# Performance work log

Hardware: AMD Instinct MI355X
Metric: run time of the kernel (lower is better)

Reference implementation:

```python
import jax, jax.numpy as jnp
import numpy as np

N_NODES = 50000
N_EDGES = 800000
H, D_IN, D_OUT = 4, 256, 64


def setup_inputs() -> dict:
    key = jax.random.key(0)
    ks = jax.random.split(key, 7)
    x = jax.random.normal(ks[0], (N_NODES, D_IN), dtype=jnp.float32)
    idx = jax.random.randint(ks[1], (2, N_EDGES), 0, N_NODES, dtype=jnp.int32)
    elem = jax.random.uniform(ks[2], (N_EDGES,), dtype=jnp.float32)
    Ws = jax.random.normal(ks[3], (H, D_IN, D_OUT), dtype=jnp.float32) * 0.05
    bs = jax.random.normal(ks[4], (H, D_OUT), dtype=jnp.float32) * 0.05
    aw = jax.random.normal(ks[5], (H, 2 * D_OUT + 1), dtype=jnp.float32) * 0.05
    ab = jax.random.normal(ks[6], (H,), dtype=jnp.float32) * 0.05
    return {"x": x, "idx": idx, "elem": elem, "Ws": Ws, "bs": bs, "aw": aw, "ab": ab}


def reference(x, idx, elem, Ws, bs, aw, ab):
    N = x.shape[0]
    O = Ws.shape[-1]
    # per-head MLP (num_mlp_layers=1 -> single Linear): [H, N, O]
    feats = jnp.einsum('nd,hdo->hno', x, Ws) + bs[:, None, :]
    # attention linear on concat(src, dst, elem): split weights instead of
    # materializing the [E, 2O+1] concat; math is identical.
    aw_src, aw_dst, aw_e = aw[:, :O], aw[:, O:2 * O], aw[:, 2 * O]
    a_s = jnp.einsum('hno,ho->hn', feats, aw_src)   # [H, N]
    a_d = jnp.einsum('hno,ho->hn', feats, aw_dst)   # [H, N]
    src, dst = idx[0], idx[1]
    score = a_s[:, src] + a_d[:, dst] + aw_e[:, None] * elem[None, :] + ab[:, None]
    w = jnp.exp(-jax.nn.relu(score / 20.0))        # [H, E], in (0, 1]
    dst_f = feats[:, dst]                          # [H, E, O] gather
    seg = lambda vals: jax.ops.segment_sum(vals, src, num_segments=N)
    pooled = jax.vmap(lambda wi, fi: seg(wi[:, None] * fi))(w, dst_f)  # [H, N, O]
    row_sum = jax.vmap(lambda wi: seg(wi))(w)                          # [H, N]
    out = pooled / row_sum[:, :, None]
    # concat heads along feature dim: [N, H*O]
    return jnp.transpose(out, (1, 0, 2)).reshape(N, H * O)
```

## Files before the change

kernel.cpp:

```cpp
#include <hip/hip_runtime.h>
#include <math.h>

constexpr int DIN = 256;
constexpr int H   = 4;
constexpr int O   = 64;
constexpr int HO  = H * O;
constexpr int AWS = 2 * O + 1;

typedef __bf16 bf16x8 __attribute__((ext_vector_type(8)));
typedef __bf16 bf16x4 __attribute__((ext_vector_type(4)));
typedef float  f32x4  __attribute__((ext_vector_type(4)));

__device__ __forceinline__ float bf2f(unsigned short u) {
    union { unsigned int i; float f; } c;
    c.i = ((unsigned int)u) << 16;
    return c.f;
}

__global__ __launch_bounds__(256) void k_prep(const float* __restrict__ Ws,
    __bf16* __restrict__ Bt, int* __restrict__ cnt, int N)
{
    const int b = blockIdx.x;
    if (b < 256) {
        const int i = b * 256 + threadIdx.x;
        const int k = i & 255;
        const int n = i >> 8;
        Bt[n * 256 + k] = (__bf16)Ws[(n >> 6) * (DIN * O) + k * O + (n & 63)];
    } else {
        const int i = (b - 256) * 256 + threadIdx.x;
        if (i < N) cnt[i] = 0;
    }
}

__global__ __launch_bounds__(256) void k_gemm_hist(const float* __restrict__ x,
    const __bf16* __restrict__ Bt, const float* __restrict__ bs,
    const float* __restrict__ aw, int N, int GB,
    __bf16* __restrict__ F, float* __restrict__ a_sT, float* __restrict__ a_dT,
    const int* __restrict__ idx, int E, int* __restrict__ cnt,
    int* __restrict__ rank)
{
    __shared__ __bf16 As[64][DIN + 8];
    const int b = blockIdx.x;
    const int t = threadIdx.x;

    if (b >= GB) {
        const int base_e = (b - GB) * 1024 + t;
        #pragma unroll
        for (int i = 0; i < 4; ++i) {
            const int e = base_e + i * 256;
            if (e < E) rank[e] = atomicAdd(&cnt[idx[e]], 1);
        }
        return;
    }

    const int w    = t >> 6;
    const int lane = t & 63;
    const int c15  = lane & 15;
    const int quad = lane >> 4;
    const int n0   = b * 64;

    #pragma unroll
    for (int i = 0; i < 16; ++i) {
        const int r   = i * 4 + w;
        const int row = n0 + r;
        float4 xv = make_float4(0.f, 0.f, 0.f, 0.f);
        if (row < N) xv = *(const float4*)&x[(size_t)row * DIN + lane * 4];
        bf16x4 pv = { (__bf16)xv.x, (__bf16)xv.y, (__bf16)xv.z, (__bf16)xv.w };
        *(bf16x4*)&As[r][lane * 4] = pv;
    }
    __syncthreads();

    f32x4 acc[4][4] = {};
    const __bf16* BtW = Bt + (size_t)(w * 64) * 256;
    const int kq = quad * 8;

    #pragma unroll
    for (int k0 = 0; k0 < DIN; k0 += 32) {
        bf16x8 afr[4], bfr[4];
        #pragma unroll
        for (int rt = 0; rt < 4; ++rt)
            afr[rt] = *(const bf16x8*)&As[rt * 16 + c15][k0 + kq];
        #pragma unroll
        for (int ct = 0; ct < 4; ++ct)
            bfr[ct] = *(const bf16x8*)&BtW[(size_t)(ct * 16 + c15) * 256 + k0 + kq];
        #pragma unroll
        for (int rt = 0; rt < 4; ++rt)
            #pragma unroll
            for (int ct = 0; ct < 4; ++ct)
                acc[rt][ct] = __builtin_amdgcn_mfma_f32_16x16x32_bf16(
                    afr[rt], bfr[ct], acc[rt][ct], 0, 0, 0);
    }

    const int h = w;
    float bsv[4], awsv[4], awdv[4];
    #pragma unroll
    for (int ct = 0; ct < 4; ++ct) {
        const int col = ct * 16 + c15;
        bsv[ct]  = bs[w * 64 + col];
        awsv[ct] = aw[h * AWS + col];
        awdv[ct] = aw[h * AWS + O + col];
    }

    #pragma unroll
    for (int rt = 0; rt < 4; ++rt) {
        float psum[4] = {0.f, 0.f, 0.f, 0.f};
        float pdum[4] = {0.f, 0.f, 0.f, 0.f};
        #pragma unroll
        for (int ct = 0; ct < 4; ++ct) {
            #pragma unroll
            for (int reg = 0; reg < 4; ++reg) {
                const float f = acc[rt][ct][reg] + bsv[ct];
                const int row = n0 + rt * 16 + quad * 4 + reg;
                if (row < N)
                    F[(size_t)row * HO + w * 64 + ct * 16 + c15] = (__bf16)f;
                psum[reg] = fmaf(f, awsv[ct], psum[reg]);
                pdum[reg] = fmaf(f, awdv[ct], pdum[reg]);
            }
        }
        #pragma unroll
        for (int reg = 0; reg < 4; ++reg) {
            float v = psum[reg], u = pdum[reg];
            #pragma unroll
            for (int off = 1; off < 16; off <<= 1) {
                v += __shfl_xor(v, off, 64);
                u += __shfl_xor(u, off, 64);
            }
            const int row = n0 + rt * 16 + quad * 4 + reg;
            if (c15 == 0 && row < N) {
                a_sT[row * H + h] = v;
                a_dT[row * H + h] = u;
            }
        }
    }
}

__global__ __launch_bounds__(256) void k_scan1(const int* __restrict__ cnt,
    int* __restrict__ row_ptr, int* __restrict__ bsum, int N)
{
    __shared__ int wsum[4], woff[4];
    const int t = threadIdx.x, b = blockIdx.x;
    const int i = b * 256 + t;
    const int lane = t & 63, w = t >> 6;

    const int v = (i < N) ? cnt[i] : 0;
    int s = v;
    #pragma unroll
    for (int off = 1; off < 64; off <<= 1) {
        int u = __shfl_up(s, off, 64);
        if (lane >= off) s += u;
    }
    if (lane == 63) wsum[w] = s;
    __syncthreads();
    if (t == 0) {
        int run = 0;
        #pragma unroll
        for (int j = 0; j < 4; ++j) { woff[j] = run; run += wsum[j]; }
        bsum[b] = run;
    }
    __syncthreads();
    const int excl = s - v + woff[w];
    if (i < N) row_ptr[i] = excl;
    if (i == N - 1) row_ptr[N] = excl + v;
}

__global__ __launch_bounds__(256) void k_scan2(int* __restrict__ bsum, int nb)
{
    __shared__ int wsum[4], woff[4];
    const int t = threadIdx.x;
    const int lane = t & 63, w = t >> 6;

    const int v = (t < nb) ? bsum[t] : 0;
    int s = v;
    #pragma unroll
    for (int off = 1; off < 64; off <<= 1) {
        int u = __shfl_up(s, off, 64);
        if (lane >= off) s += u;
    }
    if (lane == 63) wsum[w] = s;
    __syncthreads();
    if (t == 0) {
        int run = 0;
        #pragma unroll
        for (int j = 0; j < 4; ++j) { woff[j] = run; run += wsum[j]; }
    }
    __syncthreads();
    const int excl = s - v + woff[w];
    __syncthreads();
    if (t < nb) bsum[t] = excl;
    if (t == 0) bsum[nb] = woff[3] + wsum[3];
}

__global__ __launch_bounds__(256) void k_scatter(const int* __restrict__ idx,
    const float* __restrict__ elem, const int* __restrict__ rank,
    const int* __restrict__ row_ptr, const int* __restrict__ bsum, int E,
    int2* __restrict__ csr)
{
    int e = blockIdx.x * 256 + threadIdx.x;
    if (e >= E) return;
    const int s = idx[e];
    const int d = idx[E + e];
    const int pos = row_ptr[s] + bsum[s >> 8] + rank[e];
    csr[pos] = make_int2(d, __float_as_int(elem[e]));
}

__global__ __launch_bounds__(256) void k_gather(const int* __restrict__ row_ptr,
    const int* __restrict__ bsum, const int2* __restrict__ csr,
    const float* __restrict__ a_sT, const float* __restrict__ a_dT,
    const float* __restrict__ aw, const float* __restrict__ ab,
    const __bf16* __restrict__ F, float* __restrict__ out, int N)
{
    __shared__ int2  s_rec[4][64];
    __shared__ float s_w[4][256];

    const int t    = threadIdx.x;
    const int wv   = t >> 6;
    const int lane = t & 63;
    const int n    = blockIdx.x * 4 + wv;
    if (n >= N) return;
    const int h16  = lane >> 4;

    const int beg = row_ptr[n]     + bsum[n >> 8];
    const int end = row_ptr[n + 1] + bsum[(n + 1) >> 8];

    const float4 as4 = *(const float4*)&a_sT[n * 4];
    const float4 ab4 = *(const float4*)&ab[0];
    const float4 awe4 = make_float4(aw[0 * AWS + 2 * O], aw[1 * AWS + 2 * O],
                                    aw[2 * AWS + 2 * O], aw[3 * AWS + 2 * O]);

    float4 acc = make_float4(0.f, 0.f, 0.f, 0.f);
    float  rs  = 0.f;
    const __bf16* __restrict__ Fl = F + lane * 4;

    for (int base = beg; base < end; base += 64) {
        const int cnt = min(64, end - base);
        if (lane < cnt) {
            const int2 r = csr[base + lane];
            s_rec[wv][lane] = r;
            const float el = __int_as_float(r.y);
            const float4 ad = *(const float4*)&a_dT[r.x * 4];
            float4 w4;
            w4.x = __expf(-fmaxf((as4.x + ad.x + awe4.x * el + ab4.x) * 0.05f, 0.f));
            w4.y = __expf(-fmaxf((as4.y + ad.y + awe4.y * el + ab4.y) * 0.05f, 0.f));
            w4.z = __expf(-fmaxf((as4.z + ad.z + awe4.z * el + ab4.z) * 0.05f, 0.f));
            w4.w = __expf(-fmaxf((as4.w + ad.w + awe4.w * el + ab4.w) * 0.05f, 0.f));
            *(float4*)&s_w[wv][lane * 4] = w4;
        }
        __threadfence_block();

        int j = 0;
        for (; j + 4 <= cnt; j += 4) {
            const int d0 = s_rec[wv][j + 0].x;
            const int d1 = s_rec[wv][j + 1].x;
            const int d2 = s_rec[wv][j + 2].x;
            const int d3 = s_rec[wv][j + 3].x;
            const float w0 = s_w[wv][(j + 0) * 4 + h16];
            const float w1 = s_w[wv][(j + 1) * 4 + h16];
            const float w2 = s_w[wv][(j + 2) * 4 + h16];
            const float w3 = s_w[wv][(j + 3) * 4 + h16];
            const ushort4 f0 = *(const ushort4*)&Fl[(size_t)d0 * HO];
            const ushort4 f1 = *(const ushort4*)&Fl[(size_t)d1 * HO];
            const ushort4 f2 = *(const ushort4*)&Fl[(size_t)d2 * HO];
            const ushort4 f3 = *(const ushort4*)&Fl[(size_t)d3 * HO];
            acc.x = fmaf(w0, bf2f(f0.x), acc.x);
            acc.y = fmaf(w0, bf2f(f0.y), acc.y);
            acc.z = fmaf(w0, bf2f(f0.z), acc.z);
            acc.w = fmaf(w0, bf2f(f0.w), acc.w);
            acc.x = fmaf(w1, bf2f(f1.x), acc.x);
            acc.y = fmaf(w1, bf2f(f1.y), acc.y);
            acc.z = fmaf(w1, bf2f(f1.z), acc.z);
            acc.w = fmaf(w1, bf2f(f1.w), acc.w);
            acc.x = fmaf(w2, bf2f(f2.x), acc.x);
            acc.y = fmaf(w2, bf2f(f2.y), acc.y);
            acc.z = fmaf(w2, bf2f(f2.z), acc.z);
            acc.w = fmaf(w2, bf2f(f2.w), acc.w);
            acc.x = fmaf(w3, bf2f(f3.x), acc.x);
            acc.y = fmaf(w3, bf2f(f3.y), acc.y);
            acc.z = fmaf(w3, bf2f(f3.z), acc.z);
            acc.w = fmaf(w3, bf2f(f3.w), acc.w);
            rs += w0 + w1 + w2 + w3;
        }
        for (; j < cnt; ++j) {
            const int d = s_rec[wv][j].x;
            const float w = s_w[wv][j * 4 + h16];
            const ushort4 fv = *(const ushort4*)&Fl[(size_t)d * HO];
            acc.x = fmaf(w, bf2f(fv.x), acc.x);
            acc.y = fmaf(w, bf2f(fv.y), acc.y);
            acc.z = fmaf(w, bf2f(fv.z), acc.z);
            acc.w = fmaf(w, bf2f(fv.w), acc.w);
            rs += w;
        }
    }

    const float inv = 1.f / rs;
    float4 o = make_float4(acc.x * inv, acc.y * inv, acc.z * inv, acc.w * inv);
    *(float4*)&out[(size_t)n * HO + lane * 4] = o;
}

extern "C" void kernel_launch(void* const* d_in, const int* in_sizes, int n_in,
                              void* d_out, int out_size, void* d_ws, size_t ws_size,
                              hipStream_t stream)
{
    const float* x    = (const float*)d_in[0];
    const int*   idx  = (const int*)d_in[1];
    const float* elem = (const float*)d_in[2];
    const float* Ws   = (const float*)d_in[3];
    const float* bs   = (const float*)d_in[4];
    const float* aw   = (const float*)d_in[5];
    const float* ab   = (const float*)d_in[6];

    const int N = in_sizes[0] / DIN;
    const int E = in_sizes[1] / 2;
    const int nb = (N + 255) / 256;
    const int GB = (N + 63) / 64;
    const int HB = (E + 1023) / 1024;

    __bf16* F      = (__bf16*)d_ws;
    float* a_sT    = (float*)(F + (size_t)N * HO);
    float* a_dT    = a_sT + (size_t)N * H;
    int*   cnt     = (int*)(a_dT + (size_t)N * H);
    int*   row_ptr = cnt + N;
    int*   rank    = row_ptr + (N + 1);
    int*   bsum    = rank + E;
    size_t off = (size_t)((char*)(bsum + nb + 1) - (char*)d_ws);
    off = (off + 7) & ~(size_t)7;
    int2*  csr     = (int2*)((char*)d_ws + off);
    __bf16* Bt     = (__bf16*)(csr + E);
    float* out     = (float*)d_out;

    k_prep<<<256 + nb, 256, 0, stream>>>(Ws, Bt, cnt, N);
    k_gemm_hist<<<GB + HB, 256, 0, stream>>>(x, Bt, bs, aw, N, GB,
                                             F, a_sT, a_dT, idx, E, cnt, rank);
    k_scan1<<<nb, 256, 0, stream>>>(cnt, row_ptr, bsum, N);
    k_scan2<<<1, 256, 0, stream>>>(bsum, nb);
    k_scatter<<<(E + 255) / 256, 256, 0, stream>>>(idx, elem, rank, row_ptr,
                                                   bsum, E, csr);
    k_gather<<<(N + 3) / 4, 256, 0, stream>>>(row_ptr, bsum, csr, a_sT, a_dT,
                                              aw, ab, F, out, N);
}
```

Baseline: 261.6 us.

## Replace global-atomic CSR build with two-level bucketed radix sort using LDS histograms

Replaces the per-edge global atomic counting sort with a two-level scheme. Per-block LDS histograms are built over 64-node bins, then a bin-major scan and a coarse scatter run, and a per-bin LDS sort finishes the CSR. This removes heavy global atomic contention on the count array and yields a final row_ptr with no bsum correction in the gather. In exchange it adds a kernel and an extra pass over the edge records. It also packs src and dst into 16 bits each and truncates bins at CAP=3072 records, which can silently break for larger graphs or skewed degree.

```diff
diff --git a/kernel.cpp b/kernel.cpp
--- a/kernel.cpp
+++ b/kernel.cpp
@@ -6,6 +6,8 @@
 constexpr int O   = 64;
 constexpr int HO  = H * O;
 constexpr int AWS = 2 * O + 1;
+constexpr int CAP = 3072;
+constexpr int HEB = 4096;
 
 typedef __bf16 bf16x8 __attribute__((ext_vector_type(8)));
 typedef __bf16 bf16x4 __attribute__((ext_vector_type(4)));
@@ -18,38 +20,44 @@
 }
 
 __global__ __launch_bounds__(256) void k_prep(const float* __restrict__ Ws,
-    __bf16* __restrict__ Bt, int* __restrict__ cnt, int N)
-{
-    const int b = blockIdx.x;
-    if (b < 256) {
-        const int i = b * 256 + threadIdx.x;
-        const int k = i & 255;
-        const int n = i >> 8;
-        Bt[n * 256 + k] = (__bf16)Ws[(n >> 6) * (DIN * O) + k * O + (n & 63)];
-    } else {
-        const int i = (b - 256) * 256 + threadIdx.x;
-        if (i < N) cnt[i] = 0;
-    }
+    __bf16* __restrict__ Bt)
+{
+    const int i = blockIdx.x * 256 + threadIdx.x;
+    const int k = i & 255;
+    const int n = i >> 8;
+    Bt[n * 256 + k] = (__bf16)Ws[(n >> 6) * (DIN * O) + k * O + (n & 63)];
 }
 
 __global__ __launch_bounds__(256) void k_gemm_hist(const float* __restrict__ x,
     const __bf16* __restrict__ Bt, const float* __restrict__ bs,
     const float* __restrict__ aw, int N, int GB,
     __bf16* __restrict__ F, float* __restrict__ a_sT, float* __restrict__ a_dT,
-    const int* __restrict__ idx, int E, int* __restrict__ cnt,
-    int* __restrict__ rank)
-{
-    __shared__ __bf16 As[64][DIN + 8];
+    const int* __restrict__ idx, int E, int* __restrict__ rank,
+    int* __restrict__ hist, int NB, int NBIN)
+{
+    __shared__ union SM {
+        __bf16 As[64][DIN + 8];
+        int    lhist[64 * (DIN + 8) / 2];
+    } sm;
     const int b = blockIdx.x;
     const int t = threadIdx.x;
 
     if (b >= GB) {
-        const int base_e = (b - GB) * 1024 + t;
-        #pragma unroll
-        for (int i = 0; i < 4; ++i) {
+        for (int k = t; k < NBIN; k += 256) sm.lhist[k] = 0;
+        __syncthreads();
+        const int base_e = (b - GB) * HEB + t;
+        #pragma unroll
+        for (int i = 0; i < HEB / 256; ++i) {
             const int e = base_e + i * 256;
-            if (e < E) rank[e] = atomicAdd(&cnt[idx[e]], 1);
-        }
+            if (e < E) {
+                const int s = idx[e];
+                rank[e] = atomicAdd(&sm.lhist[s >> 6], 1);
+            }
+        }
+        __syncthreads();
+        const int bh = b - GB;
+        for (int k = t; k < NBIN; k += 256)
+            hist[(size_t)k * NB + bh] = sm.lhist[k];
         return;
     }
 
@@ -66,7 +74,7 @@
         float4 xv = make_float4(0.f, 0.f, 0.f, 0.f);
         if (row < N) xv = *(const float4*)&x[(size_t)row * DIN + lane * 4];
         bf16x4 pv = { (__bf16)xv.x, (__bf16)xv.y, (__bf16)xv.z, (__bf16)xv.w };
-        *(bf16x4*)&As[r][lane * 4] = pv;
+        *(bf16x4*)&sm.As[r][lane * 4] = pv;
     }
     __syncthreads();
 
@@ -79,7 +87,7 @@
         bf16x8 afr[4], bfr[4];
         #pragma unroll
         for (int rt = 0; rt < 4; ++rt)
-            afr[rt] = *(const bf16x8*)&As[rt * 16 + c15][k0 + kq];
+            afr[rt] = *(const bf16x8*)&sm.As[rt * 16 + c15][k0 + kq];
         #pragma unroll
         for (int ct = 0; ct < 4; ++ct)
             bfr[ct] = *(const bf16x8*)&BtW[(size_t)(ct * 16 + c15) * 256 + k0 + kq];
@@ -134,19 +142,26 @@
     }
 }
 
-__global__ __launch_bounds__(256) void k_scan1(const int* __restrict__ cnt,
-    int* __restrict__ row_ptr, int* __restrict__ bsum, int N)
+__global__ __launch_bounds__(256) void k_scan1(int* __restrict__ data,
+    int* __restrict__ bsum, int T)
 {
     __shared__ int wsum[4], woff[4];
     const int t = threadIdx.x, b = blockIdx.x;
-    const int i = b * 256 + t;
     const int lane = t & 63, w = t >> 6;
-
-    const int v = (i < N) ? cnt[i] : 0;
-    int s = v;
+    const int i0 = b * 1024 + t * 4;
+
+    int4 v = make_int4(0, 0, 0, 0);
+    if (i0 + 3 < T) v = *(const int4*)&data[i0];
+    else {
+        if (i0     < T) v.x = data[i0];
+        if (i0 + 1 < T) v.y = data[i0 + 1];
+        if (i0 + 2 < T) v.z = data[i0 + 2];
+    }
+    const int tot = v.x + v.y + v.z + v.w;
+    int s = tot;
     #pragma unroll
     for (int off = 1; off < 64; off <<= 1) {
-        int u = __shfl_up(s, off, 64);
+        const int u = __shfl_up(s, off, 64);
         if (lane >= off) s += u;
     }
     if (lane == 63) wsum[w] = s;
@@ -158,22 +173,36 @@
         bsum[b] = run;
     }
     __syncthreads();
-    const int excl = s - v + woff[w];
-    if (i < N) row_ptr[i] = excl;
-    if (i == N - 1) row_ptr[N] = excl + v;
-}
-
-__global__ __launch_bounds__(256) void k_scan2(int* __restrict__ bsum, int nb)
+    const int e0 = s - tot + woff[w];
+    int4 o;
+    o.x = e0; o.y = e0 + v.x; o.z = o.y + v.y; o.w = o.z + v.z;
+    if (i0 + 3 < T) *(int4*)&data[i0] = o;
+    else {
+        if (i0     < T) data[i0]     = o.x;
+        if (i0 + 1 < T) data[i0 + 1] = o.y;
+        if (i0 + 2 < T) data[i0 + 2] = o.z;
+    }
+}
+
+__global__ __launch_bounds__(256) void k_scan2(int* __restrict__ data, int n)
 {
     __shared__ int wsum[4], woff[4];
     const int t = threadIdx.x;
     const int lane = t & 63, w = t >> 6;
-
-    const int v = (t < nb) ? bsum[t] : 0;
-    int s = v;
+    const int i0 = t * 4;
+
+    int4 v = make_int4(0, 0, 0, 0);
+    if (i0 + 3 < n) v = *(const int4*)&data[i0];
+    else {
+        if (i0     < n) v.x = data[i0];
+        if (i0 + 1 < n) v.y = data[i0 + 1];
+        if (i0 + 2 < n) v.z = data[i0 + 2];
+    }
+    const int tot = v.x + v.y + v.z + v.w;
+    int s = tot;
     #pragma unroll
     for (int off = 1; off < 64; off <<= 1) {
-        int u = __shfl_up(s, off, 64);
+        const int u = __shfl_up(s, off, 64);
         if (lane >= off) s += u;
     }
     if (lane == 63) wsum[w] = s;
@@ -184,30 +213,87 @@
         for (int j = 0; j < 4; ++j) { woff[j] = run; run += wsum[j]; }
     }
     __syncthreads();
-    const int excl = s - v + woff[w];
-    __syncthreads();
-    if (t < nb) bsum[t] = excl;
-    if (t == 0) bsum[nb] = woff[3] + wsum[3];
+    const int e0 = s - tot + woff[w];
+    int4 o;
+    o.x = e0; o.y = e0 + v.x; o.z = o.y + v.y; o.w = o.z + v.z;
+    if (i0 + 3 < n) *(int4*)&data[i0] = o;
+    else {
+        if (i0     < n) data[i0]     = o.x;
+        if (i0 + 1 < n) data[i0 + 1] = o.y;
+        if (i0 + 2 < n) data[i0 + 2] = o.z;
+    }
 }
 
 __global__ __launch_bounds__(256) void k_scatter(const int* __restrict__ idx,
     const float* __restrict__ elem, const int* __restrict__ rank,
-    const int* __restrict__ row_ptr, const int* __restrict__ bsum, int E,
-    int2* __restrict__ csr)
-{
-    int e = blockIdx.x * 256 + threadIdx.x;
+    const int* __restrict__ hist, const int* __restrict__ hsum,
+    int NB, int E, int2* __restrict__ csr)
+{
+    const int e = blockIdx.x * 256 + threadIdx.x;
     if (e >= E) return;
     const int s = idx[e];
     const int d = idx[E + e];
-    const int pos = row_ptr[s] + bsum[s >> 8] + rank[e];
-    csr[pos] = make_int2(d, __float_as_int(elem[e]));
+    const int i = (s >> 6) * NB + (e / HEB);
+    const int pos = hist[i] + hsum[i >> 10] + rank[e];
+    csr[pos] = make_int2((int)(((unsigned)s << 16) | (unsigned)d),
+                         __float_as_int(elem[e]));
+}
+
+__global__ __launch_bounds__(256) void k_binsort(const int* __restrict__ hist,
+    const int* __restrict__ hsum, int NB, int NBIN, int N, int E,
+    int* __restrict__ row_ptr, int2* __restrict__ csr)
+{
+    __shared__ int2 recs[CAP];
+    __shared__ int h[64];
+    __shared__ int cur[64];
+    const int k = blockIdx.x;
+    const int t = threadIdx.x;
+
+    const int i0 = k * NB;
+    const int S = hist[i0] + hsum[i0 >> 10];
+    int Snext = E;
+    if (k + 1 < NBIN) {
+        const int i1 = (k + 1) * NB;
+        Snext = hist[i1] + hsum[i1 >> 10];
+    }
+    int cnt = Snext - S;
+    if (cnt > CAP) cnt = CAP;
+
+    if (t < 64) h[t] = 0;
+    __syncthreads();
+    for (int j = t; j < cnt; j += 256) {
+        const int2 r = csr[S + j];
+        recs[j] = r;
+        atomicAdd(&h[((unsigned)r.x >> 16) & 63], 1);
+    }
+    __syncthreads();
+    if (t < 64) {
+        const int v = h[t];
+        int s = v;
+        #pragma unroll
+        for (int off = 1; off < 64; off <<= 1) {
+            const int u = __shfl_up(s, off, 64);
+            if (t >= off) s += u;
+        }
+        const int excl = s - v;
+        const int node = k * 64 + t;
+        if (node < N)     row_ptr[node] = S + excl;
+        if (node == N - 1) row_ptr[N]   = S + excl + v;
+        cur[t] = S + excl;
+    }
+    __syncthreads();
+    for (int j = t; j < cnt; j += 256) {
+        const int2 r = recs[j];
+        const int pos = atomicAdd(&cur[((unsigned)r.x >> 16) & 63], 1);
+        csr[pos] = make_int2((int)((unsigned)r.x & 0xFFFFu), r.y);
+    }
 }
 
 __global__ __launch_bounds__(256) void k_gather(const int* __restrict__ row_ptr,
-    const int* __restrict__ bsum, const int2* __restrict__ csr,
-    const float* __restrict__ a_sT, const float* __restrict__ a_dT,
-    const float* __restrict__ aw, const float* __restrict__ ab,
-    const __bf16* __restrict__ F, float* __restrict__ out, int N)
+    const int2* __restrict__ csr, const float* __restrict__ a_sT,
+    const float* __restrict__ a_dT, const float* __restrict__ aw,
+    const float* __restrict__ ab, const __bf16* __restrict__ F,
+    float* __restrict__ out, int N)
 {
     __shared__ int2  s_rec[4][64];
     __shared__ float s_w[4][256];
@@ -219,8 +305,8 @@
     if (n >= N) return;
     const int h16  = lane >> 4;
 
-    const int beg = row_ptr[n]     + bsum[n >> 8];
-    const int end = row_ptr[n + 1] + bsum[(n + 1) >> 8];
+    const int beg = row_ptr[n];
+    const int end = row_ptr[n + 1];
 
     const float4 as4 = *(const float4*)&a_sT[n * 4];
     const float4 ab4 = *(const float4*)&ab[0];
@@ -308,32 +394,37 @@
     const float* aw   = (const float*)d_in[5];
     const float* ab   = (const float*)d_in[6];
 
-    const int N = in_sizes[0] / DIN;
-    const int E = in_sizes[1] / 2;
-    const int nb = (N + 255) / 256;
-    const int GB = (N + 63) / 64;
-    const int HB = (E + 1023) / 1024;
+    const int N    = in_sizes[0] / DIN;
+    const int E    = in_sizes[1] / 2;
+    const int GB   = (N + 63) / 64;
+    const int NB   = (E + HEB - 1) / HEB;
+    const int NBIN = (N + 63) / 64;
+    const int T    = NBIN * NB;
+    const int nb1  = (T + 1023) / 1024;
 
     __bf16* F      = (__bf16*)d_ws;
     float* a_sT    = (float*)(F + (size_t)N * HO);
     float* a_dT    = a_sT + (size_t)N * H;
-    int*   cnt     = (int*)(a_dT + (size_t)N * H);
-    int*   row_ptr = cnt + N;
+    int*   hist    = (int*)(a_dT + (size_t)N * H);
+    int*   hsum    = hist + T;
+    int*   row_ptr = hsum + (nb1 + 1);
     int*   rank    = row_ptr + (N + 1);
-    int*   bsum    = rank + E;
-    size_t off = (size_t)((char*)(bsum + nb + 1) - (char*)d_ws);
-    off = (off + 7) & ~(size_t)7;
+    size_t off = (size_t)((char*)(rank + E) - (char*)d_ws);
+    off = (off + 15) & ~(size_t)15;
     int2*  csr     = (int2*)((char*)d_ws + off);
     __bf16* Bt     = (__bf16*)(csr + E);
     float* out     = (float*)d_out;
 
-    k_prep<<<256 + nb, 256, 0, stream>>>(Ws, Bt, cnt, N);
-    k_gemm_hist<<<GB + HB, 256, 0, stream>>>(x, Bt, bs, aw, N, GB,
-                                             F, a_sT, a_dT, idx, E, cnt, rank);
-    k_scan1<<<nb, 256, 0, stream>>>(cnt, row_ptr, bsum, N);
-    k_scan2<<<1, 256, 0, stream>>>(bsum, nb);
-    k_scatter<<<(E + 255) / 256, 256, 0, stream>>>(idx, elem, rank, row_ptr,
-                                                   bsum, E, csr);
-    k_gather<<<(N + 3) / 4, 256, 0, stream>>>(row_ptr, bsum, csr, a_sT, a_dT,
+    k_prep<<<256, 256, 0, stream>>>(Ws, Bt);
+    k_gemm_hist<<<GB + NB, 256, 0, stream>>>(x, Bt, bs, aw, N, GB,
+                                             F, a_sT, a_dT, idx, E,
+                                             rank, hist, NB, NBIN);
+    k_scan1<<<nb1, 256, 0, stream>>>(hist, hsum, T);
+    k_scan2<<<1, 256, 0, stream>>>(hsum, nb1);
+    k_scatter<<<(E + 255) / 256, 256, 0, stream>>>(idx, elem, rank, hist,
+                                                   hsum, NB, E, csr);
+    k_binsort<<<NBIN, 256, 0, stream>>>(hist, hsum, NB, NBIN, N, E,
+                                        row_ptr, csr);
+    k_gather<<<(N + 3) / 4, 256, 0, stream>>>(row_ptr, csr, a_sT, a_dT,
                                               aw, ab, F, out, N);
 }
```

Result: faster. 240.3 us (-8.1%).
